# Performance work log

Hardware: AMD Instinct MI355X
Metric: run time of the kernel (lower is better)

## Reference

```python
import jax, jax.numpy as jnp
import numpy as np

B, S, D, H = 4, 2048, 1024, 16
HD = D // H


def setup_inputs() -> dict:
    key = jax.random.key(0)
    ks = jax.random.split(key, 5)
    scale = 1.0 / np.sqrt(D)
    return {
        "x": jax.random.normal(ks[0], (B, S, D), dtype=jnp.float32),
        "W_q": jax.random.normal(ks[1], (D, D), dtype=jnp.float32) * scale,
        "W_k": jax.random.normal(ks[2], (D, D), dtype=jnp.float32) * scale,
        "W_v": jax.random.normal(ks[3], (D, D), dtype=jnp.float32) * scale,
        "W_o": jax.random.normal(ks[4], (D, D), dtype=jnp.float32) * scale,
    }


def reference(x, W_q, W_k, W_v, W_o):
    # Linear with weight [out, in]: y = x @ W^T
    def proj(W):
        return jnp.einsum('bsd,ed->bshf', x, W.reshape(H, HD, D).transpose(0, 1, 2).reshape(D, D)) if False else (x @ W.T).reshape(B, S, H, HD).transpose(0, 2, 1, 3)

    q = proj(W_q)  # [B, H, S, HD]
    k = proj(W_k)
    v = proj(W_v)

    scores = jnp.einsum('bhqd,bhkd->bhqk', q, k) / jnp.sqrt(jnp.float32(HD))
    causal = jnp.triu(jnp.ones((S, S), dtype=bool), k=1)  # True above diagonal -> masked
    scores = jnp.where(causal, -jnp.inf, scores)
    probs = jax.nn.softmax(scores, axis=-1)
    out = jnp.einsum('bhqk,bhkd->bhqd', probs, v)  # [B, H, S, HD]
    out = out.transpose(0, 2, 1, 3).reshape(B, S, D)
    return out @ W_o.T
```

## Files before the change

### kernel.cpp

```cpp
#include <hip/hip_runtime.h>
#include <cstdint>
#include <cstddef>

typedef unsigned short u16;
typedef __attribute__((ext_vector_type(8))) short short8;
typedef __attribute__((ext_vector_type(4))) short short4v;
typedef __attribute__((ext_vector_type(8))) unsigned short ushort8v;
typedef __attribute__((ext_vector_type(4))) unsigned short ushort4v;
typedef __attribute__((ext_vector_type(4))) unsigned int uint4v;
typedef __attribute__((ext_vector_type(4))) float f32x4;

#define QSCALE 0.18033688011112042f
#define THR_L2 11.5417f


__device__ __forceinline__ u16 f2bf(float f) {
  unsigned int u = __builtin_bit_cast(unsigned int, f);
  u += 0x7FFFu + ((u >> 16) & 1u);
  return (u16)(u >> 16);
}

__device__ __forceinline__ void async16(const void* g, void* l) {
  __builtin_amdgcn_global_load_lds(
      (const __attribute__((address_space(1))) unsigned int*)g,
      (__attribute__((address_space(3))) unsigned int*)l, 16, 0, 0);
}

__device__ __forceinline__ float fmax3(float a, float b, float c) {
  float r;
  asm("v_max3_f32 %0, %1, %2, %3" : "=v"(r) : "v"(a), "v"(b), "v"(c));
  return r;
}

__device__ __forceinline__ unsigned int cvtpk(float lo, float hi) {
  unsigned int r;
  asm("v_cvt_pk_bf16_f32 %0, %1, %2" : "=v"(r) : "v"(lo), "v"(hi));
  return r;
}


__global__ void cvt_all(const float* __restrict__ x, const float* __restrict__ Wq,
                        const float* __restrict__ Wk, const float* __restrict__ Wv,
                        const float* __restrict__ Wo, u16* __restrict__ out) {
  const int bid = blockIdx.x;
  const float* src;
  int i;
  size_t doff;
  if (bid < 8192) {
    i = bid * 1024 + threadIdx.x * 4;
    src = x;
    doff = (size_t)i;
  } else {
    const int k = bid - 8192;
    const int wsel = k >> 10;
    i = (k & 1023) * 1024 + threadIdx.x * 4;
    src = (wsel == 0) ? Wq : (wsel == 1) ? Wk : (wsel == 2) ? Wv : Wo;
    doff = 8388608 + (size_t)wsel * 1048576 + i;
  }
  float4 v = *(const float4*)(src + i);
  ushort4v o;
  o[0] = f2bf(v.x); o[1] = f2bf(v.y); o[2] = f2bf(v.z); o[3] = f2bf(v.w);
  *(ushort4v*)(out + doff) = o;
}


template<int MODE>
__global__ __launch_bounds__(512, 1) void gemm_qb(
    const u16* __restrict__ A, const u16* __restrict__ Bw,
    void* __restrict__ Cout, int M, int N, int K)
{
  const int t = threadIdx.x;
  const int lane = t & 63, w = t >> 6;
  const int li = lane & 15, g = lane >> 4;
  const int wm = w >> 1, wn = w & 1;

  const int nx = gridDim.x;
  const int hwid = blockIdx.y * nx + blockIdx.x;
  const int cpx = (nx * gridDim.y) >> 3;
  const int lid = (hwid & 7) * cpx + (hwid >> 3);
  const int brow = (lid / nx) * 256, bcol = (lid % nx) * 128;

  __shared__ u16 As[4][256 * 32];
  __shared__ u16 Bs[4][128 * 32];

  f32x4 acc[4][4];
#pragma unroll
  for (int i = 0; i < 4; ++i)
#pragma unroll
    for (int j = 0; j < 4; ++j) acc[i][j] = f32x4{0.f, 0.f, 0.f, 0.f};

  auto STAGE = [&](int T) {
    const int b = T & 3;
    const int k0 = T * 32;
#pragma unroll
    for (int L = 0; L < 2; ++L) {
      const int f2 = t + 512 * L;
      const int row = f2 >> 2;
      const int cb = ((f2 & 3) * 16) ^ (((row >> 1) & 3) << 4);
      async16(A + (size_t)(brow + row) * K + k0 + (cb >> 1), &As[b][f2 * 8]);
    }
    const int rowb = t >> 2;
    const int cbb = ((t & 3) * 16) ^ (((rowb >> 1) & 3) << 4);
    async16(Bw + (size_t)(bcol + rowb) * K + k0 + (cbb >> 1), &Bs[b][t * 8]);
  };

  STAGE(0); STAGE(1); STAGE(2);

  const int NT = K >> 5;
  const int ksw = (g * 8) ^ (((li >> 1) & 3) << 3);

#pragma unroll 1
  for (int T = 0; T < NT; ++T) {
    if (T < NT - 2)      asm volatile("s_waitcnt vmcnt(6)" ::: "memory");
    else if (T == NT - 2) asm volatile("s_waitcnt vmcnt(3)" ::: "memory");
    else                  asm volatile("s_waitcnt vmcnt(0)" ::: "memory");
    asm volatile("s_barrier" ::: "memory");
    const int b = T & 3;
    short8 af[4], bfr[4];
#pragma unroll
    for (int mt = 0; mt < 4; ++mt)
      af[mt] = *(const short8*)&As[b][(wm * 64 + mt * 16 + li) * 32 + ksw];
#pragma unroll
    for (int nt = 0; nt < 4; ++nt)
      bfr[nt] = *(const short8*)&Bs[b][(wn * 64 + nt * 16 + li) * 32 + ksw];

    if (T + 3 < NT) STAGE(T + 3);

    __builtin_amdgcn_s_setprio(1);
#pragma unroll
    for (int mt = 0; mt < 4; ++mt)
#pragma unroll
      for (int nt = 0; nt < 4; ++nt)
        acc[mt][nt] = __builtin_amdgcn_mfma_f32_16x16x32_bf16(af[mt], bfr[nt], acc[mt][nt], 0, 0, 0);
    __builtin_amdgcn_s_setprio(0);
  }

#pragma unroll
  for (int mt = 0; mt < 4; ++mt)
#pragma unroll
    for (int nt = 0; nt < 4; ++nt) {
      const int col = bcol + wn * 64 + nt * 16 + li;
#pragma unroll
      for (int r = 0; r < 4; ++r) {
        const int row = brow + wm * 64 + mt * 16 + g * 4 + r;
        float v = acc[mt][nt][r];
        if (MODE == 0) {
          const int which = col >> 10;
          const int c2 = col & 1023;
          if (which == 0) v *= QSCALE;
          const int bb = row >> 11, s = row & 2047;
          const int h = c2 >> 6, hd = c2 & 63;
          ((u16*)Cout)[(size_t)which * 8388608 +
                       (((size_t)(bb * 16 + h) * 2048) + s) * 64 + hd] = f2bf(v);
        } else {
          ((float*)Cout)[(size_t)row * N + col] = v;
        }
      }
    }
}


__global__ __launch_bounds__(256) void transpose_hd_s(
    const u16* __restrict__ V, u16* __restrict__ VT)
{
  const int sb = blockIdx.x;
  const int bh = blockIdx.y;
  __shared__ u16 tile[64 * 72];
  const int t = threadIdx.x;
  const int r = t >> 3;
  const int c8 = (t & 7) * 8;
  const size_t base = (size_t)bh * 2048 * 64;
#pragma unroll
  for (int half = 0; half < 2; ++half) {
    const int row = r + 32 * half;
    ushort8v v = *(const ushort8v*)(V + base + (size_t)(sb * 64 + row) * 64 + c8);
    *(ushort8v*)&tile[row * 72 + c8] = v;
  }
  __syncthreads();
#pragma unroll
  for (int half = 0; half < 2; ++half) {
    const int hd = r + 32 * half;
    ushort8v o;
#pragma unroll
    for (int j = 0; j < 8; ++j) o[j] = tile[(c8 + j) * 72 + hd];
    *(ushort8v*)(VT + base + (size_t)hd * 2048 + sb * 64 + c8) = o;
  }
}


__global__ __launch_bounds__(256, 2) void flash_attn3(
    const u16* __restrict__ Qp, const u16* __restrict__ Kp,
    const u16* __restrict__ VTp, u16* __restrict__ Oattn)
{
  const int hwid = blockIdx.x;
  const int lid = (hwid & 7) * 64 + (hwid >> 3);
  const int pr = lid & 7, bh = lid >> 3;

  const int t = threadIdx.x;
  const int lane = t & 63, w = t >> 6;
  const int li = lane & 15, g = lane >> 4;

  __shared__ u16 Kl[3][64 * 64];
  __shared__ u16 Vl[3][64 * 64];

  const size_t bh_off = (size_t)bh * (2048 * 64);
  const int tile0 = pr, tile1 = 15 - pr;
  const int njb0 = 2 * tile0 + 2;

  short8 qf0[2][2], qf1[2][2];
#pragma unroll
  for (int qs = 0; qs < 2; ++qs) {
    const u16* qp0 = Qp + bh_off + (size_t)(tile0 * 128 + qs * 64 + w * 16 + li) * 64 + g * 8;
    qf0[qs][0] = *(const short8*)qp0;
    qf0[qs][1] = *(const short8*)(qp0 + 32);
    const u16* qp1 = Qp + bh_off + (size_t)(tile1 * 128 + qs * 64 + w * 16 + li) * 64 + g * 8;
    qf1[qs][0] = *(const short8*)qp1;
    qf1[qs][1] = *(const short8*)(qp1 + 32);
  }
  short8 qc[2][2];
#pragma unroll
  for (int qs = 0; qs < 2; ++qs) { qc[qs][0] = qf0[qs][0]; qc[qs][1] = qf0[qs][1]; }

  int qbase = tile0 * 128;

  f32x4 o_acc[2][4];
#pragma unroll
  for (int qs = 0; qs < 2; ++qs)
#pragma unroll
    for (int i = 0; i < 4; ++i) o_acc[qs][i] = f32x4{0.f, 0.f, 0.f, 0.f};
  float m_i[2] = {-1e30f, -1e30f};
  float l_i[2] = {0.f, 0.f};

  const int b = bh >> 4, h = bh & 15;
  const int ksw = (li & 7) << 3;

  auto STAGE = [&](int i, int s) {
    const int jb = (i < njb0) ? i : (i - njb0);
#pragma unroll
    for (int L = 0; L < 2; ++L) {
      const int f = t + 256 * L;
      const int kbyte = (f * 16) ^ (((f >> 3) & 7) << 4);
      async16(Kp + bh_off + (size_t)jb * 4096 + (kbyte >> 1),
              &Kl[s][(w * 64 + 256 * L) * 8]);
      const int vrow = f >> 3;
      const int vb = ((f & 7) * 16) ^ ((vrow & 7) << 4);
      async16(VTp + bh_off + (size_t)vrow * 2048 + jb * 64 + (vb >> 1),
              &Vl[s][(w * 64 + 256 * L) * 8]);
    }
  };

  auto WRITEO = [&]() {
#pragma unroll
    for (int qs = 0; qs < 2; ++qs) {
      const float inv_l = 1.f / l_i[qs];
      const int qrow = qbase + qs * 64 + w * 16 + li;
      u16* op = Oattn + ((size_t)(b * 2048 + qrow)) * 1024 + h * 64;
#pragma unroll
      for (int dt = 0; dt < 4; ++dt) {
        ushort4v st;
#pragma unroll
        for (int r = 0; r < 4; ++r) st[r] = f2bf(o_acc[qs][dt][r] * inv_l);
        *(ushort4v*)(op + dt * 16 + g * 4) = st;
      }
    }
  };

  STAGE(0, 0);
  STAGE(1, 1);
  asm volatile("s_waitcnt vmcnt(4)" ::: "memory");
  __builtin_amdgcn_s_barrier();

#pragma unroll 1
  for (int i = 0; i < 34; ++i) {
    const int s = i % 3;
    if (i + 2 < 34) STAGE(i + 2, (i + 2) % 3);

    const int jb = (i < njb0) ? i : (i - njb0);
    const u16* __restrict__ Ks = &Kl[s][0];
    const u16* __restrict__ Vs = &Vl[s][0];

    f32x4 s_acc[2][4];
#pragma unroll
    for (int qs = 0; qs < 2; ++qs)
#pragma unroll
      for (int jt = 0; jt < 4; ++jt) s_acc[qs][jt] = f32x4{0.f, 0.f, 0.f, 0.f};
    __builtin_amdgcn_s_setprio(1);
#pragma unroll
    for (int kc = 0; kc < 2; ++kc)
#pragma unroll
      for (int jt = 0; jt < 4; ++jt) {
        short8 kf = *(const short8*)&Ks[(jt * 16 + li) * 64 + ((kc * 32 + g * 8) ^ ksw)];
        s_acc[0][jt] = __builtin_amdgcn_mfma_f32_16x16x32_bf16(kf, qc[0][kc], s_acc[0][jt], 0, 0, 0);
        s_acc[1][jt] = __builtin_amdgcn_mfma_f32_16x16x32_bf16(kf, qc[1][kc], s_acc[1][jt], 0, 0, 0);
      }
    __builtin_amdgcn_s_setprio(0);

    float mx[2];
    bool need = false;
#pragma unroll
    for (int qs = 0; qs < 2; ++qs) {
      if (jb * 64 + 63 > qbase + qs * 64 + w * 16) {
        const int tq = qbase + qs * 64 + w * 16 + li - jb * 64;
#pragma unroll
        for (int jt = 0; jt < 4; ++jt)
#pragma unroll
          for (int r = 0; r < 4; ++r)
            if (jt * 16 + g * 4 + r > tq) s_acc[qs][jt][r] = -1e30f;
      }
      float t0 = fmax3(s_acc[qs][0][0], s_acc[qs][0][1], s_acc[qs][0][2]);
      float t1 = fmax3(s_acc[qs][0][3], s_acc[qs][1][0], s_acc[qs][1][1]);
      float t2 = fmax3(s_acc[qs][1][2], s_acc[qs][1][3], s_acc[qs][2][0]);
      float t3 = fmax3(s_acc[qs][2][1], s_acc[qs][2][2], s_acc[qs][2][3]);
      float t4m = fmax3(s_acc[qs][3][0], s_acc[qs][3][1], s_acc[qs][3][2]);
      float m01 = fmax3(t0, t1, s_acc[qs][3][3]);
      float m23 = fmax3(t2, t3, t4m);
      float mm = fmaxf(m01, m23);
      mm = fmaxf(mm, __shfl_xor(mm, 16));
      mm = fmaxf(mm, __shfl_xor(mm, 32));
      mx[qs] = mm;
      need = need || (mm > m_i[qs] + THR_L2);
    }

    if (__any((int)need)) {
#pragma unroll
      for (int qs = 0; qs < 2; ++qs) {
        const float mn = fmaxf(m_i[qs], mx[qs]);
        const float corr = __builtin_amdgcn_exp2f(m_i[qs] - mn);
        l_i[qs] *= corr;
#pragma unroll
        for (int dt = 0; dt < 4; ++dt) o_acc[qs][dt] *= corr;
        m_i[qs] = mn;
      }
    }

    short8 pf[2][2];
#pragma unroll
    for (int qs = 0; qs < 2; ++qs) {
      const float mi = m_i[qs];
      float ps = 0.f;
#pragma unroll
      for (int jt = 0; jt < 4; ++jt)
#pragma unroll
        for (int r = 0; r < 4; ++r) {
          float e = __builtin_amdgcn_exp2f(s_acc[qs][jt][r] - mi);
          s_acc[qs][jt][r] = e;
          ps += e;
        }
      ps += __shfl_xor(ps, 16);
      ps += __shfl_xor(ps, 32);
      l_i[qs] += ps;
#pragma unroll
      for (int kc = 0; kc < 2; ++kc) {
        uint4v u;
        u[0] = cvtpk(s_acc[qs][2 * kc][0], s_acc[qs][2 * kc][1]);
        u[1] = cvtpk(s_acc[qs][2 * kc][2], s_acc[qs][2 * kc][3]);
        u[2] = cvtpk(s_acc[qs][2 * kc + 1][0], s_acc[qs][2 * kc + 1][1]);
        u[3] = cvtpk(s_acc[qs][2 * kc + 1][2], s_acc[qs][2 * kc + 1][3]);
        pf[qs][kc] = __builtin_bit_cast(short8, u);
      }
    }

    __builtin_amdgcn_s_setprio(1);
#pragma unroll
    for (int kc = 0; kc < 2; ++kc)
#pragma unroll
      for (int dt = 0; dt < 4; ++dt) {
        const int rowb = (dt * 16 + li) * 64;
        short4v v0 = *(const short4v*)&Vs[rowb + ((kc * 32 + g * 4) ^ ksw)];
        short4v v1 = *(const short4v*)&Vs[rowb + ((kc * 32 + 16 + g * 4) ^ ksw)];
        short8 vf = __builtin_shufflevector(v0, v1, 0, 1, 2, 3, 4, 5, 6, 7);
        o_acc[0][dt] = __builtin_amdgcn_mfma_f32_16x16x32_bf16(vf, pf[0][kc], o_acc[0][dt], 0, 0, 0);
        o_acc[1][dt] = __builtin_amdgcn_mfma_f32_16x16x32_bf16(vf, pf[1][kc], o_acc[1][dt], 0, 0, 0);
      }
    __builtin_amdgcn_s_setprio(0);

    asm volatile("s_waitcnt lgkmcnt(0)" ::: "memory");
    if (i < 32) { asm volatile("s_waitcnt vmcnt(4)" ::: "memory"); }
    else        { asm volatile("s_waitcnt vmcnt(0)" ::: "memory"); }
    __builtin_amdgcn_s_barrier();

    if (i == njb0 - 1) {
      WRITEO();
      qbase = tile1 * 128;
#pragma unroll
      for (int qs = 0; qs < 2; ++qs) {
        qc[qs][0] = qf1[qs][0]; qc[qs][1] = qf1[qs][1];
        m_i[qs] = -1e30f; l_i[qs] = 0.f;
#pragma unroll
        for (int dt = 0; dt < 4; ++dt) o_acc[qs][dt] = f32x4{0.f, 0.f, 0.f, 0.f};
      }
    }
  }

  WRITEO();
}


extern "C" void kernel_launch(void* const* d_in, const int* in_sizes, int n_in,
                              void* d_out, int out_size, void* d_ws, size_t ws_size,
                              hipStream_t stream) {
  const float* x  = (const float*)d_in[0];
  const float* Wq = (const float*)d_in[1];
  const float* Wk = (const float*)d_in[2];
  const float* Wv = (const float*)d_in[3];
  const float* Wo = (const float*)d_in[4];

  const size_t NX = 8388608;
  const size_t NW = 1048576;

  u16* xb  = (u16*)d_ws;
  u16* wqb = xb + NX;
  u16* wob = wqb + 3 * NW;
  u16* Qb  = wob + NW;
  u16* Kb  = Qb + NX;
  u16* Vb  = Kb + NX;
  u16* VTb = Vb + NX;
  u16* attnb = Vb;

  cvt_all<<<12288, 256, 0, stream>>>(x, Wq, Wk, Wv, Wo, xb);

  gemm_qb<0><<<dim3(24, 32), 512, 0, stream>>>(xb, wqb, Qb, 8192, 3072, 1024);

  transpose_hd_s<<<dim3(32, 64), 256, 0, stream>>>(Vb, VTb);
  flash_attn3<<<512, 256, 0, stream>>>(Qb, Kb, VTb, attnb);

  gemm_qb<1><<<dim3(8, 32), 512, 0, stream>>>(attnb, wob, d_out, 8192, 1024, 1024);
}
```

Measured before the change: 176.5 us.

## Permute V transpose layout for single 128-bit LDS reads; compute row sums via MFMA

```diff
diff --git a/kernel.cpp b/kernel.cpp
--- a/kernel.cpp
+++ b/kernel.cpp
@@ -182,13 +182,17 @@
     const int hd = r + 32 * half;
     ushort8v o;
 #pragma unroll
-    for (int j = 0; j < 8; ++j) o[j] = tile[(c8 + j) * 72 + hd];
+    for (int j = 0; j < 8; ++j) {
+      const int pos = c8 + j;
+      const int kv = (pos & 32) + (((pos >> 2) & 1) << 4) + (((pos >> 3) & 3) << 2) + (pos & 3);
+      o[j] = tile[kv * 72 + hd];
+    }
     *(ushort8v*)(VT + base + (size_t)hd * 2048 + sb * 64 + c8) = o;
   }
 }
 
 
-__global__ __launch_bounds__(256, 2) void flash_attn3(
+__global__ __launch_bounds__(256, 2) void flash_attn9(
     const u16* __restrict__ Qp, const u16* __restrict__ Kp,
     const u16* __restrict__ VTp, u16* __restrict__ Oattn)
 {
@@ -223,13 +227,19 @@
 
   int qbase = tile0 * 128;
 
+  short8 onesf;
+#pragma unroll
+  for (int j = 0; j < 8; ++j) onesf[j] = (short)0x3F80;
+
   f32x4 o_acc[2][4];
-#pragma unroll
-  for (int qs = 0; qs < 2; ++qs)
+  f32x4 osum[2];
+#pragma unroll
+  for (int qs = 0; qs < 2; ++qs) {
+    osum[qs] = f32x4{0.f, 0.f, 0.f, 0.f};
 #pragma unroll
     for (int i = 0; i < 4; ++i) o_acc[qs][i] = f32x4{0.f, 0.f, 0.f, 0.f};
+  }
   float m_i[2] = {-1e30f, -1e30f};
-  float l_i[2] = {0.f, 0.f};
 
   const int b = bh >> 4, h = bh & 15;
   const int ksw = (li & 7) << 3;
@@ -252,7 +262,7 @@
   auto WRITEO = [&]() {
 #pragma unroll
     for (int qs = 0; qs < 2; ++qs) {
-      const float inv_l = 1.f / l_i[qs];
+      const float inv_l = 1.f / osum[qs][0];
       const int qrow = qbase + qs * 64 + w * 16 + li;
       u16* op = Oattn + ((size_t)(b * 2048 + qrow)) * 1024 + h * 64;
 #pragma unroll
@@ -326,7 +336,7 @@
       for (int qs = 0; qs < 2; ++qs) {
         const float mn = fmaxf(m_i[qs], mx[qs]);
         const float corr = __builtin_amdgcn_exp2f(m_i[qs] - mn);
-        l_i[qs] *= corr;
+        osum[qs] *= corr;
 #pragma unroll
         for (int dt = 0; dt < 4; ++dt) o_acc[qs][dt] *= corr;
         m_i[qs] = mn;
@@ -337,18 +347,11 @@
 #pragma unroll
     for (int qs = 0; qs < 2; ++qs) {
       const float mi = m_i[qs];
-      float ps = 0.f;
 #pragma unroll
       for (int jt = 0; jt < 4; ++jt)
 #pragma unroll
-        for (int r = 0; r < 4; ++r) {
-          float e = __builtin_amdgcn_exp2f(s_acc[qs][jt][r] - mi);
-          s_acc[qs][jt][r] = e;
-          ps += e;
-        }
-      ps += __shfl_xor(ps, 16);
-      ps += __shfl_xor(ps, 32);
-      l_i[qs] += ps;
+        for (int r = 0; r < 4; ++r)
+          s_acc[qs][jt][r] = __builtin_amdgcn_exp2f(s_acc[qs][jt][r] - mi);
 #pragma unroll
       for (int kc = 0; kc < 2; ++kc) {
         uint4v u;
@@ -362,16 +365,16 @@
 
     __builtin_amdgcn_s_setprio(1);
 #pragma unroll
-    for (int kc = 0; kc < 2; ++kc)
+    for (int kc = 0; kc < 2; ++kc) {
+      osum[0] = __builtin_amdgcn_mfma_f32_16x16x32_bf16(onesf, pf[0][kc], osum[0], 0, 0, 0);
+      osum[1] = __builtin_amdgcn_mfma_f32_16x16x32_bf16(onesf, pf[1][kc], osum[1], 0, 0, 0);
 #pragma unroll
       for (int dt = 0; dt < 4; ++dt) {
-        const int rowb = (dt * 16 + li) * 64;
-        short4v v0 = *(const short4v*)&Vs[rowb + ((kc * 32 + g * 4) ^ ksw)];
-        short4v v1 = *(const short4v*)&Vs[rowb + ((kc * 32 + 16 + g * 4) ^ ksw)];
-        short8 vf = __builtin_shufflevector(v0, v1, 0, 1, 2, 3, 4, 5, 6, 7);
+        short8 vf = *(const short8*)&Vs[(dt * 16 + li) * 64 + ((kc * 32 + g * 8) ^ ksw)];
         o_acc[0][dt] = __builtin_amdgcn_mfma_f32_16x16x32_bf16(vf, pf[0][kc], o_acc[0][dt], 0, 0, 0);
         o_acc[1][dt] = __builtin_amdgcn_mfma_f32_16x16x32_bf16(vf, pf[1][kc], o_acc[1][dt], 0, 0, 0);
       }
+    }
     __builtin_amdgcn_s_setprio(0);
 
     asm volatile("s_waitcnt lgkmcnt(0)" ::: "memory");
@@ -385,7 +388,8 @@
 #pragma unroll
       for (int qs = 0; qs < 2; ++qs) {
         qc[qs][0] = qf1[qs][0]; qc[qs][1] = qf1[qs][1];
-        m_i[qs] = -1e30f; l_i[qs] = 0.f;
+        m_i[qs] = -1e30f;
+        osum[qs] = f32x4{0.f, 0.f, 0.f, 0.f};
 #pragma unroll
         for (int dt = 0; dt < 4; ++dt) o_acc[qs][dt] = f32x4{0.f, 0.f, 0.f, 0.f};
       }
@@ -422,7 +426,7 @@
   gemm_qb<0><<<dim3(24, 32), 512, 0, stream>>>(xb, wqb, Qb, 8192, 3072, 1024);
 
   transpose_hd_s<<<dim3(32, 64), 256, 0, stream>>>(Vb, VTb);
-  flash_attn3<<<512, 256, 0, stream>>>(Qb, Kb, VTb, attnb);
+  flash_attn9<<<512, 256, 0, stream>>>(Qb, Kb, VTb, attnb);
 
   gemm_qb<1><<<dim3(8, 32), 512, 0, stream>>>(attnb, wob, d_out, 8192, 1024, 1024);
 }
```

New measurement: 167.5 us. -5.1%, faster.
